# Optimization experiments

Measured on AMD Instinct MI355X. Metric: run time of the kernel, lower is better.

The kernel has to match this reference:

```python
import jax, jax.numpy as jnp
import numpy as np

N_NODES = 50000
N_EDGES = 800000
D = 128  # in_dim == hidden_dim


def setup_inputs() -> dict:
    key = jax.random.key(0)
    k1, k2, k3, k4 = jax.random.split(key, 4)
    x = jax.random.normal(k1, (N_NODES, D), dtype=jnp.float32)
    edge_index = jax.random.randint(k2, (2, N_EDGES), 0, N_NODES, dtype=jnp.int64)
    # Glorot-ish scale for square weights
    scale = 1.0 / np.sqrt(D)
    W1 = jax.random.normal(k3, (D, D), dtype=jnp.float32) * scale
    W2 = jax.random.normal(k4, (D, D), dtype=jnp.float32) * scale
    b1 = jnp.zeros((D,), dtype=jnp.float32)
    b2 = jnp.zeros((D,), dtype=jnp.float32)
    return {"x": x, "edge_index": edge_index, "W1": W1, "b1": b1, "W2": W2, "b2": b2}


def _gcn_layer(x, W, b, src, dst, norm, n):
    # PyG GCNConv: h = x @ W, then symmetric-normalized scatter-add, then + bias
    h = x @ W                                   # [N, D] dense GEMM
    msg = h[src] * norm[:, None]                # [E', D] gather + scale
    out = jax.ops.segment_sum(msg, dst, num_segments=n)  # scatter-add
    return out + b


def reference(x, edge_index, W1, b1, W2, b2):
    n = x.shape[0]
    # add self-loops (GCNConv default add_self_loops=True)
    loops = jnp.arange(n, dtype=edge_index.dtype)
    src = jnp.concatenate([edge_index[0], loops])
    dst = jnp.concatenate([edge_index[1], loops])
    # symmetric normalization: deg^{-1/2}[src] * deg^{-1/2}[dst]
    deg = jax.ops.segment_sum(jnp.ones_like(src, dtype=x.dtype), dst, num_segments=n)
    dinv = jax.lax.rsqrt(jnp.maximum(deg, 1.0))  # deg >= 1 due to self-loops
    norm = dinv[src] * dinv[dst]
    # layer 1: conv -> relu (dropout is identity in eval mode)
    h = jax.nn.relu(_gcn_layer(x, W1, b1, src, dst, norm, n))
    # layer 2 (cut='c2'): conv -> relu
    h = jax.nn.relu(_gcn_layer(h, W2, b2, src, dst, norm, n))
    return h
```

## Files before the change

### kernel.cpp

```cpp
#include <hip/hip_runtime.h>

#define NN 50000
#define NE 800000
#define DD 128
#define NSTRIP 3125
#define NB 196
#define CHUNK 4096
#define MAXB 6144

#define OF_BCNT  0
#define OF_BBASE 256
#define OF_BCUR  768
#define OF_DINV  1024
#define OF_OFFS  51200
#define OF_TMP   101632
#define OF_CSRU  901632
#define OF_G     1301632
#define OF_X2    4501632
#define OF_W1H   10901632
#define OF_W1L   10909824
#define OF_W2H   10918016
#define OF_W2L   10926208

typedef __attribute__((ext_vector_type(8))) short bf8_t;
typedef __attribute__((ext_vector_type(8))) unsigned short us8;
typedef __attribute__((ext_vector_type(4))) float f32x4;

static __device__ __forceinline__ unsigned short f2bf(float f) {
    unsigned int u = __float_as_uint(f);
    unsigned int r = (u + 0x7fffu + ((u >> 16) & 1u)) >> 16;
    return (unsigned short)r;
}
static __device__ __forceinline__ float bf2f(unsigned short h) {
    return __uint_as_float(((unsigned int)h) << 16);
}

__global__ void k_wconv(const float* __restrict__ W1, const float* __restrict__ W2,
                        ushort* __restrict__ w1h, ushort* __restrict__ w1l,
                        ushort* __restrict__ w2h, ushort* __restrict__ w2l,
                        int* __restrict__ bcnt) {
    if (blockIdx.x == 0) bcnt[threadIdx.x] = 0;
    int gg = blockIdx.x * 256 + threadIdx.x;
    const float* W = (gg < 2048) ? W1 : W2;
    ushort* wh = (gg < 2048) ? w1h : w2h;
    ushort* wl = (gg < 2048) ? w1l : w2l;
    int g = gg & 2047;
    int ntile = g >> 8;
    int kk = (g >> 6) & 3;
    int lane = g & 63;
    int k0 = kk * 32 + ((lane >> 4) * 8);
    int col = ntile * 16 + (lane & 15);
#pragma unroll
    for (int j = 0; j < 8; ++j) {
        float w = W[(k0 + j) * DD + col];
        unsigned short h = f2bf(w);
        wh[(size_t)g * 8 + j] = h;
        wl[(size_t)g * 8 + j] = f2bf(w - bf2f(h));
    }
}

__global__ void k_hist(const int* __restrict__ dst, int* __restrict__ bcnt) {
    __shared__ int lc[256];
    int tid = threadIdx.x;
    lc[tid] = 0;
    __syncthreads();
    int e0 = blockIdx.x * CHUNK;
    int e1 = e0 + CHUNK; if (e1 > NE) e1 = NE;
    for (int e = e0 + tid; e < e1; e += 256)
        atomicAdd(&lc[dst[e] >> 8], 1);
    __syncthreads();
    if (lc[tid]) atomicAdd(&bcnt[tid], lc[tid]);
}

__global__ void k_bscan(const int* __restrict__ bcnt, int* __restrict__ bbase,
                        int* __restrict__ bcur, int* __restrict__ offs) {
    __shared__ int sh[256];
    int tid = threadIdx.x;
    int v = bcnt[tid];
    sh[tid] = v;
    __syncthreads();
    for (int o = 1; o < 256; o <<= 1) {
        int t = (tid >= o) ? sh[tid - o] : 0;
        __syncthreads();
        sh[tid] += t;
        __syncthreads();
    }
    bbase[tid] = sh[tid] - v;
    bcur[tid]  = sh[tid] - v;
    if (tid == 255) bbase[256] = sh[255];
    if (tid == 0) offs[NN] = NE;
}

__global__ void k_shuf(const int* __restrict__ src, const int* __restrict__ dst,
                       int* __restrict__ bcur, unsigned int* __restrict__ tmp) {
    __shared__ int lcnt[256];
    __shared__ int lbase[256];
    __shared__ int lcur[256];
    int tid = threadIdx.x;
    lcnt[tid] = 0;
    __syncthreads();
    int e0 = blockIdx.x * CHUNK;
    int e1 = e0 + CHUNK; if (e1 > NE) e1 = NE;
    for (int e = e0 + tid; e < e1; e += 256)
        atomicAdd(&lcnt[dst[e] >> 8], 1);
    __syncthreads();
    if (lcnt[tid]) lbase[tid] = atomicAdd(&bcur[tid], lcnt[tid]);
    lcur[tid] = 0;
    __syncthreads();
    for (int e = e0 + tid; e < e1; e += 256) {
        int d = dst[e], s = src[e];
        int b = d >> 8;
        int r = atomicAdd(&lcur[b], 1);
        tmp[lbase[b] + r] = ((unsigned int)s << 8) | (unsigned int)(d & 255);
    }
}

__global__ __launch_bounds__(256) void k_sort(const int* __restrict__ bbase,
                                              const unsigned int* __restrict__ tmp,
                                              ushort* __restrict__ csru,
                                              int* __restrict__ offs,
                                              float* __restrict__ dinv) {
    __shared__ unsigned int ent[MAXB];
    __shared__ int cnt[256];
    __shared__ int boff[256];
    __shared__ int cur[256];
    int b = blockIdx.x, tid = threadIdx.x;
    int base = bbase[b];
    int nb = bbase[b + 1] - base;
    cnt[tid] = 0;
    __syncthreads();
    for (int i = tid; i < nb; i += 256) {
        unsigned int v = tmp[base + i];
        ent[i] = v;
        atomicAdd(&cnt[v & 255], 1);
    }
    __syncthreads();
    int v = cnt[tid];
    boff[tid] = v;
    __syncthreads();
    for (int o = 1; o < 256; o <<= 1) {
        int t = (tid >= o) ? boff[tid - o] : 0;
        __syncthreads();
        boff[tid] += t;
        __syncthreads();
    }
    int excl = boff[tid] - v;
    int node = b * 256 + tid;
    if (node < NN) {
        offs[node] = base + excl;
        dinv[node] = rsqrtf((float)(v + 1));
    }
    cur[tid] = excl;
    __syncthreads();
    for (int i = tid; i < nb; i += 256) {
        unsigned int e = ent[i];
        int bin = e & 255;
        int r = atomicAdd(&cur[bin], 1);
        csru[base + r] = (ushort)(e >> 8);
    }
}

__global__ __launch_bounds__(256) void k_mgemm(const float* __restrict__ X,
                                               const ushort* __restrict__ wh,
                                               const ushort* __restrict__ wl,
                                               const float* __restrict__ dinv,
                                               ushort* __restrict__ G) {
    int wave = threadIdx.x >> 6;
    int lane = threadIdx.x & 63;
    int strip = blockIdx.x * 4 + wave;
    if (strip >= NSTRIP) return;
    int rb = strip << 4;
    int m = lane & 15;
    int quad = lane >> 4;
    const float* ar = X + (size_t)(rb + m) * DD;
    f32x4 acc[8];
#pragma unroll
    for (int t = 0; t < 8; ++t) acc[t] = (f32x4){0.f, 0.f, 0.f, 0.f};
#pragma unroll
    for (int kk = 0; kk < 4; ++kk) {
        float4 xa = *(const float4*)(ar + kk * 32 + quad * 8);
        float4 xb = *(const float4*)(ar + kk * 32 + quad * 8 + 4);
        float xs[8] = {xa.x, xa.y, xa.z, xa.w, xb.x, xb.y, xb.z, xb.w};
        bf8_t ah, al;
#pragma unroll
        for (int j = 0; j < 8; ++j) {
            unsigned short hh = f2bf(xs[j]);
            ah[j] = (short)hh;
            al[j] = (short)f2bf(xs[j] - bf2f(hh));
        }
#pragma unroll
        for (int t = 0; t < 8; ++t) {
            size_t bo = ((size_t)(t * 4 + kk) * 64 + lane) * 8;
            bf8_t bh = *(const bf8_t*)(wh + bo);
            bf8_t bl = *(const bf8_t*)(wl + bo);
            acc[t] = __builtin_amdgcn_mfma_f32_16x16x32_bf16(ah, bh, acc[t], 0, 0, 0);
            acc[t] = __builtin_amdgcn_mfma_f32_16x16x32_bf16(ah, bl, acc[t], 0, 0, 0);
            acc[t] = __builtin_amdgcn_mfma_f32_16x16x32_bf16(al, bh, acc[t], 0, 0, 0);
        }
    }
    float dv[4];
#pragma unroll
    for (int r = 0; r < 4; ++r) dv[r] = dinv[rb + quad * 4 + r];
#pragma unroll
    for (int t = 0; t < 8; ++t) {
#pragma unroll
        for (int r = 0; r < 4; ++r)
            G[(size_t)(rb + quad * 4 + r) * DD + t * 16 + m] = f2bf(dv[r] * acc[t][r]);
    }
}

__global__ void k_agg(const ushort* __restrict__ g, const float* __restrict__ dinv,
                      const int* __restrict__ offs, const ushort* __restrict__ csru,
                      const float* __restrict__ bias, float* __restrict__ outf) {
    int wave = threadIdx.x >> 6;
    int lane = threadIdx.x & 63;
    int node = blockIdx.x * 4 + wave;
    int q = lane >> 4;
    int l = lane & 15;
    float a0[8] = {0.f, 0.f, 0.f, 0.f, 0.f, 0.f, 0.f, 0.f};
    float a1[8] = {0.f, 0.f, 0.f, 0.f, 0.f, 0.f, 0.f, 0.f};
    int e  = offs[node] + q;
    int e1 = offs[node + 1];
    for (; e + 4 < e1; e += 8) {
        int s0 = csru[e];
        int s1 = csru[e + 4];
        us8 v0 = *(const us8*)(g + (size_t)s0 * DD + 8 * l);
        us8 v1 = *(const us8*)(g + (size_t)s1 * DD + 8 * l);
#pragma unroll
        for (int j = 0; j < 8; ++j) {
            a0[j] += bf2f(v0[j]);
            a1[j] += bf2f(v1[j]);
        }
    }
    if (e < e1) {
        int s0 = csru[e];
        us8 v0 = *(const us8*)(g + (size_t)s0 * DD + 8 * l);
#pragma unroll
        for (int j = 0; j < 8; ++j) a0[j] += bf2f(v0[j]);
    }
    if (q == 0) {
        us8 v = *(const us8*)(g + (size_t)node * DD + 8 * l);
#pragma unroll
        for (int j = 0; j < 8; ++j) a0[j] += bf2f(v[j]);
    }
#pragma unroll
    for (int j = 0; j < 8; ++j) {
        a0[j] += a1[j];
        a0[j] += __shfl_xor(a0[j], 16, 64);
        a0[j] += __shfl_xor(a0[j], 32, 64);
    }
    if (q == 0) {
        float di = dinv[node];
        float* op = outf + (size_t)node * DD + 8 * l;
        const float* bp = bias + 8 * l;
        float4 o0, o1;
        o0.x = fmaxf(di * a0[0] + bp[0], 0.f);
        o0.y = fmaxf(di * a0[1] + bp[1], 0.f);
        o0.z = fmaxf(di * a0[2] + bp[2], 0.f);
        o0.w = fmaxf(di * a0[3] + bp[3], 0.f);
        o1.x = fmaxf(di * a0[4] + bp[4], 0.f);
        o1.y = fmaxf(di * a0[5] + bp[5], 0.f);
        o1.z = fmaxf(di * a0[6] + bp[6], 0.f);
        o1.w = fmaxf(di * a0[7] + bp[7], 0.f);
        *(float4*)op = o0;
        *(float4*)(op + 4) = o1;
    }
}

extern "C" void kernel_launch(void* const* d_in, const int* in_sizes, int n_in,
                              void* d_out, int out_size, void* d_ws, size_t ws_size,
                              hipStream_t stream) {
    const float* x  = (const float*)d_in[0];
    const int*   ei = (const int*)d_in[1];
    const float* W1 = (const float*)d_in[2];
    const float* b1 = (const float*)d_in[3];
    const float* W2 = (const float*)d_in[4];
    const float* b2 = (const float*)d_in[5];
    float* out = (float*)d_out;

    const int* src = ei;
    const int* dst = ei + NE;

    int*          wsi  = (int*)d_ws;
    float*        wsf  = (float*)d_ws;
    ushort*       wsu  = (ushort*)d_ws;
    unsigned int* wsuw = (unsigned int*)d_ws;
    int*    bcnt  = wsi + OF_BCNT;
    int*    bbase = wsi + OF_BBASE;
    int*    bcur  = wsi + OF_BCUR;
    float*  dinv  = wsf + OF_DINV;
    int*    offs  = wsi + OF_OFFS;
    unsigned int* tmp = wsuw + OF_TMP;
    ushort* csru  = wsu + (size_t)OF_CSRU * 2;
    ushort* gbuf  = wsu + (size_t)OF_G * 2;
    float*  x2    = wsf + OF_X2;
    ushort* w1h   = wsu + (size_t)OF_W1H * 2;
    ushort* w1l   = wsu + (size_t)OF_W1L * 2;
    ushort* w2h   = wsu + (size_t)OF_W2H * 2;
    ushort* w2l   = wsu + (size_t)OF_W2L * 2;

    const int chunks = (NE + CHUNK - 1) / CHUNK;

    hipLaunchKernelGGL(k_wconv, dim3(16), dim3(256), 0, stream,
                       W1, W2, w1h, w1l, w2h, w2l, bcnt);
    hipLaunchKernelGGL(k_hist,  dim3(chunks), dim3(256), 0, stream, dst, bcnt);
    hipLaunchKernelGGL(k_bscan, dim3(1), dim3(256), 0, stream, bcnt, bbase, bcur, offs);
    hipLaunchKernelGGL(k_shuf,  dim3(chunks), dim3(256), 0, stream, src, dst, bcur, tmp);
    hipLaunchKernelGGL(k_sort,  dim3(NB), dim3(256), 0, stream, bbase, tmp, csru, offs, dinv);

    const int gblocks = (NSTRIP + 3) / 4;

    hipLaunchKernelGGL(k_mgemm, dim3(gblocks), dim3(256), 0, stream, x, w1h, w1l, dinv, gbuf);
    hipLaunchKernelGGL(k_agg,   dim3(NN / 4), dim3(256), 0, stream,
                       gbuf, dinv, offs, csru, b1, x2);
    hipLaunchKernelGGL(k_mgemm, dim3(gblocks), dim3(256), 0, stream, x2, w2h, w2l, dinv, gbuf);
    hipLaunchKernelGGL(k_agg,   dim3(NN / 4), dim3(256), 0, stream,
                       gbuf, dinv, offs, csru, b2, out);
}
```

Measured before the change: 217.3 us.

## Replace histogram+scan with fixed-capacity buckets and unroll aggregation to four accumulators

Removes the histogram and bucket-scan kernels by giving each destination bucket a fixed MAXB-sized slot in the temp buffer, so k_shuf appends directly with a per-bucket atomic counter. The CSR offsets become (start,end) int2 pairs because buckets are no longer contiguous. The aggregation loop is unrolled to four independent gathers per iteration to raise memory-level parallelism. This assumes no bucket exceeds MAXB edges, which holds only statistically for random inputs, and it adds padding gaps to the CSR and temp layout.

```diff
diff --git a/kernel.cpp b/kernel.cpp
--- a/kernel.cpp
+++ b/kernel.cpp
@@ -8,19 +8,17 @@
 #define CHUNK 4096
 #define MAXB 6144
 
-#define OF_BCNT  0
-#define OF_BBASE 256
-#define OF_BCUR  768
-#define OF_DINV  1024
-#define OF_OFFS  51200
-#define OF_TMP   101632
-#define OF_CSRU  901632
-#define OF_G     1301632
-#define OF_X2    4501632
-#define OF_W1H   10901632
-#define OF_W1L   10909824
-#define OF_W2H   10918016
-#define OF_W2L   10926208
+#define OF_BCUR  0
+#define OF_DINV  256
+#define OF_OFFS2 50432
+#define OF_TMP   150528
+#define OF_CSRU  1723392
+#define OF_G     2509824
+#define OF_X2    5709824
+#define OF_W1H   12109824
+#define OF_W1L   12118016
+#define OF_W2H   12126208
+#define OF_W2L   12134400
 
 typedef __attribute__((ext_vector_type(8))) short bf8_t;
 typedef __attribute__((ext_vector_type(8))) unsigned short us8;
@@ -38,8 +36,8 @@
 __global__ void k_wconv(const float* __restrict__ W1, const float* __restrict__ W2,
                         ushort* __restrict__ w1h, ushort* __restrict__ w1l,
                         ushort* __restrict__ w2h, ushort* __restrict__ w2l,
-                        int* __restrict__ bcnt) {
-    if (blockIdx.x == 0) bcnt[threadIdx.x] = 0;
+                        int* __restrict__ bcur) {
+    if (blockIdx.x == 0) bcur[threadIdx.x] = 0;
     int gg = blockIdx.x * 256 + threadIdx.x;
     const float* W = (gg < 2048) ? W1 : W2;
     ushort* wh = (gg < 2048) ? w1h : w2h;
@@ -59,38 +57,6 @@
     }
 }
 
-__global__ void k_hist(const int* __restrict__ dst, int* __restrict__ bcnt) {
-    __shared__ int lc[256];
-    int tid = threadIdx.x;
-    lc[tid] = 0;
-    __syncthreads();
-    int e0 = blockIdx.x * CHUNK;
-    int e1 = e0 + CHUNK; if (e1 > NE) e1 = NE;
-    for (int e = e0 + tid; e < e1; e += 256)
-        atomicAdd(&lc[dst[e] >> 8], 1);
-    __syncthreads();
-    if (lc[tid]) atomicAdd(&bcnt[tid], lc[tid]);
-}
-
-__global__ void k_bscan(const int* __restrict__ bcnt, int* __restrict__ bbase,
-                        int* __restrict__ bcur, int* __restrict__ offs) {
-    __shared__ int sh[256];
-    int tid = threadIdx.x;
-    int v = bcnt[tid];
-    sh[tid] = v;
-    __syncthreads();
-    for (int o = 1; o < 256; o <<= 1) {
-        int t = (tid >= o) ? sh[tid - o] : 0;
-        __syncthreads();
-        sh[tid] += t;
-        __syncthreads();
-    }
-    bbase[tid] = sh[tid] - v;
-    bcur[tid]  = sh[tid] - v;
-    if (tid == 255) bbase[256] = sh[255];
-    if (tid == 0) offs[NN] = NE;
-}
-
 __global__ void k_shuf(const int* __restrict__ src, const int* __restrict__ dst,
                        int* __restrict__ bcur, unsigned int* __restrict__ tmp) {
     __shared__ int lcnt[256];
@@ -111,22 +77,23 @@
         int d = dst[e], s = src[e];
         int b = d >> 8;
         int r = atomicAdd(&lcur[b], 1);
-        tmp[lbase[b] + r] = ((unsigned int)s << 8) | (unsigned int)(d & 255);
-    }
-}
-
-__global__ __launch_bounds__(256) void k_sort(const int* __restrict__ bbase,
+        tmp[(size_t)b * MAXB + lbase[b] + r] =
+            ((unsigned int)s << 8) | (unsigned int)(d & 255);
+    }
+}
+
+__global__ __launch_bounds__(256) void k_sort(const int* __restrict__ bcur,
                                               const unsigned int* __restrict__ tmp,
                                               ushort* __restrict__ csru,
-                                              int* __restrict__ offs,
+                                              int2* __restrict__ offs2,
                                               float* __restrict__ dinv) {
     __shared__ unsigned int ent[MAXB];
     __shared__ int cnt[256];
     __shared__ int boff[256];
     __shared__ int cur[256];
     int b = blockIdx.x, tid = threadIdx.x;
-    int base = bbase[b];
-    int nb = bbase[b + 1] - base;
+    int base = b * MAXB;
+    int nb = bcur[b];
     cnt[tid] = 0;
     __syncthreads();
     for (int i = tid; i < nb; i += 256) {
@@ -147,7 +114,7 @@
     int excl = boff[tid] - v;
     int node = b * 256 + tid;
     if (node < NN) {
-        offs[node] = base + excl;
+        offs2[node] = make_int2(base + excl, base + excl + v);
         dinv[node] = rsqrtf((float)(v + 1));
     }
     cur[tid] = excl;
@@ -210,7 +177,7 @@
 }
 
 __global__ void k_agg(const ushort* __restrict__ g, const float* __restrict__ dinv,
-                      const int* __restrict__ offs, const ushort* __restrict__ csru,
+                      const int2* __restrict__ offs2, const ushort* __restrict__ csru,
                       const float* __restrict__ bias, float* __restrict__ outf) {
     int wave = threadIdx.x >> 6;
     int lane = threadIdx.x & 63;
@@ -219,20 +186,29 @@
     int l = lane & 15;
     float a0[8] = {0.f, 0.f, 0.f, 0.f, 0.f, 0.f, 0.f, 0.f};
     float a1[8] = {0.f, 0.f, 0.f, 0.f, 0.f, 0.f, 0.f, 0.f};
-    int e  = offs[node] + q;
-    int e1 = offs[node + 1];
-    for (; e + 4 < e1; e += 8) {
+    float a2[8] = {0.f, 0.f, 0.f, 0.f, 0.f, 0.f, 0.f, 0.f};
+    float a3[8] = {0.f, 0.f, 0.f, 0.f, 0.f, 0.f, 0.f, 0.f};
+    int2 oe = offs2[node];
+    int e  = oe.x + q;
+    int e1 = oe.y;
+    for (; e + 12 < e1; e += 16) {
         int s0 = csru[e];
         int s1 = csru[e + 4];
+        int s2 = csru[e + 8];
+        int s3 = csru[e + 12];
         us8 v0 = *(const us8*)(g + (size_t)s0 * DD + 8 * l);
         us8 v1 = *(const us8*)(g + (size_t)s1 * DD + 8 * l);
+        us8 v2 = *(const us8*)(g + (size_t)s2 * DD + 8 * l);
+        us8 v3 = *(const us8*)(g + (size_t)s3 * DD + 8 * l);
 #pragma unroll
         for (int j = 0; j < 8; ++j) {
             a0[j] += bf2f(v0[j]);
             a1[j] += bf2f(v1[j]);
+            a2[j] += bf2f(v2[j]);
+            a3[j] += bf2f(v3[j]);
         }
     }
-    if (e < e1) {
+    for (; e < e1; e += 4) {
         int s0 = csru[e];
         us8 v0 = *(const us8*)(g + (size_t)s0 * DD + 8 * l);
 #pragma unroll
@@ -245,7 +221,7 @@
     }
 #pragma unroll
     for (int j = 0; j < 8; ++j) {
-        a0[j] += a1[j];
+        a0[j] += a1[j] + a2[j] + a3[j];
         a0[j] += __shfl_xor(a0[j], 16, 64);
         a0[j] += __shfl_xor(a0[j], 32, 64);
     }
@@ -285,11 +261,9 @@
     float*        wsf  = (float*)d_ws;
     ushort*       wsu  = (ushort*)d_ws;
     unsigned int* wsuw = (unsigned int*)d_ws;
-    int*    bcnt  = wsi + OF_BCNT;
-    int*    bbase = wsi + OF_BBASE;
     int*    bcur  = wsi + OF_BCUR;
     float*  dinv  = wsf + OF_DINV;
-    int*    offs  = wsi + OF_OFFS;
+    int2*   offs2 = (int2*)(wsi + OF_OFFS2);
     unsigned int* tmp = wsuw + OF_TMP;
     ushort* csru  = wsu + (size_t)OF_CSRU * 2;
     ushort* gbuf  = wsu + (size_t)OF_G * 2;
@@ -302,18 +276,16 @@
     const int chunks = (NE + CHUNK - 1) / CHUNK;
 
     hipLaunchKernelGGL(k_wconv, dim3(16), dim3(256), 0, stream,
-                       W1, W2, w1h, w1l, w2h, w2l, bcnt);
-    hipLaunchKernelGGL(k_hist,  dim3(chunks), dim3(256), 0, stream, dst, bcnt);
-    hipLaunchKernelGGL(k_bscan, dim3(1), dim3(256), 0, stream, bcnt, bbase, bcur, offs);
+                       W1, W2, w1h, w1l, w2h, w2l, bcur);
     hipLaunchKernelGGL(k_shuf,  dim3(chunks), dim3(256), 0, stream, src, dst, bcur, tmp);
-    hipLaunchKernelGGL(k_sort,  dim3(NB), dim3(256), 0, stream, bbase, tmp, csru, offs, dinv);
+    hipLaunchKernelGGL(k_sort,  dim3(NB), dim3(256), 0, stream, bcur, tmp, csru, offs2, dinv);
 
     const int gblocks = (NSTRIP + 3) / 4;
 
     hipLaunchKernelGGL(k_mgemm, dim3(gblocks), dim3(256), 0, stream, x, w1h, w1l, dinv, gbuf);
     hipLaunchKernelGGL(k_agg,   dim3(NN / 4), dim3(256), 0, stream,
-                       gbuf, dinv, offs, csru, b1, x2);
+                       gbuf, dinv, offs2, csru, b1, x2);
     hipLaunchKernelGGL(k_mgemm, dim3(gblocks), dim3(256), 0, stream, x2, w2h, w2l, dinv, gbuf);
     hipLaunchKernelGGL(k_agg,   dim3(NN / 4), dim3(256), 0, stream,
-                       gbuf, dinv, offs, csru, b2, out);
-}
+                       gbuf, dinv, offs2, csru, b2, out);
+}
```

Result: no change. 219.6 us (+1.0%).
